# Kernel optimization log

Measured on AMD Instinct MI355X. Metric: run time of the kernel, lower is better.

The kernel has to match this reference:

```python
import jax, jax.numpy as jnp
import numpy as np

TOP_K = 8


def setup_inputs() -> dict:
    key = jax.random.key(0)
    k1, k2 = jax.random.split(key)
    N, D, E = 16384, 4096, 64
    x = jax.random.normal(k1, (N, D), dtype=jnp.float32)
    W = jax.random.normal(k2, (E, D), dtype=jnp.float32) * (1.0 / np.sqrt(D))
    b = jnp.zeros((E,), dtype=jnp.float32)
    return {"x": x, "W": W, "b": b}


def reference(x, W, b):
    # gate: [N, E]
    logits = jnp.einsum('nd,ed->ne', x, W) + b
    top_vals, top_idx = jax.lax.top_k(logits, TOP_K)  # [N, k]
    N = logits.shape[0]
    rows = jnp.arange(N)[:, None]  # [N, 1] broadcast against [N, k]
    neg_inf = jnp.full_like(logits, -jnp.inf)
    sparse = neg_inf.at[rows, top_idx].set(top_vals)
    sparse_logits = jax.nn.softmax(sparse, axis=-1)  # non-topk entries -> 0
    return (sparse_logits, top_idx)
```

## Files before the change

### kernel.cpp

```cpp
#include <hip/hip_runtime.h>
#include <cfloat>
#include <cmath>

#define M     16384
#define K     4096
#define E     64
#define TOPK  8
#define GAP_THRESH 1e-4f

#define RCAP  2048
#define FKS   8

typedef __attribute__((ext_vector_type(8))) short bf16x8;
typedef __attribute__((ext_vector_type(4))) short s16x4;
typedef __attribute__((ext_vector_type(4))) float f32x4;


__device__ __forceinline__ short f2bf(float f) {
    unsigned u = __builtin_bit_cast(unsigned, f);
    u += 0x7FFFu + ((u >> 16) & 1u);
    return (short)(u >> 16);
}
__device__ __forceinline__ float bf2f(short h) {
    unsigned u = ((unsigned)(unsigned short)h) << 16;
    return __builtin_bit_cast(float, u);
}

__global__ __launch_bounds__(256) void prep_kernel(const float* __restrict__ W,
                                                   short* __restrict__ Whf,
                                                   short* __restrict__ Wlf,
                                                   int* __restrict__ count) {
    int t = blockIdx.x * 256 + threadIdx.x;
    float w = W[t];
    short h = f2bf(w);
    short lo = f2bf(w - bf2f(h));
    int e = t >> 12, k = t & 4095;
    int gc = k >> 5, kk = k & 31;
    size_t fidx = (((size_t)gc * 4 + (e >> 4)) * 64 + (kk >> 3) * 16 + (e & 15)) * 8
                  + (kk & 7);
    Whf[fidx] = h;
    Wlf[fidx] = lo;
    if (t == 0) *count = 0;
}

__device__ __forceinline__ void mfma3(const bf16x8& ah, const bf16x8& al,
                                      const bf16x8& wh, const bf16x8& wl,
                                      f32x4& acc) {
    acc = __builtin_amdgcn_mfma_f32_16x16x32_bf16(ah, wh, acc, 0, 0, 0);
    acc = __builtin_amdgcn_mfma_f32_16x16x32_bf16(ah, wl, acc, 0, 0, 0);
    acc = __builtin_amdgcn_mfma_f32_16x16x32_bf16(al, wh, acc, 0, 0, 0);
}

__global__ __launch_bounds__(256) void gate_kernel(
    const float* __restrict__ x,
    const short* __restrict__ Whf,
    const short* __restrict__ Wlf,
    const float* __restrict__ b,
    float* __restrict__ outp,
    float* __restrict__ outi,
    int*   __restrict__ count,
    int*   __restrict__ list)
{
    __shared__ short lxh[2][16 * 128];
    __shared__ short lxl[2][16 * 128];
    __shared__ float llog[16 * E];

    const int t  = threadIdx.x;
    const int l  = t & 63;
    const int wv = t >> 6;
    const int row0 = blockIdx.x * 16;

    const int srA  = t >> 5;
    const int scol = t & 31;
    const float* gxA = x + (size_t)(row0 + srA) * K + scol * 4;
    const float* gxB = x + (size_t)(row0 + 8 + srA) * K + scol * 4;
    const int pu   = (scol >> 1) ^ (srA & 7);
    const int offA = srA * 128 + pu * 8 + (scol & 1) * 4;
    const int offB = (8 + srA) * 128 + pu * 8 + (scol & 1) * 4;

#define CVTW(nb, v, off) do {                                          \
        s16x4 hh_, ll_;                                                \
        float vv_[4] = {(v).x, (v).y, (v).z, (v).w};                   \
        _Pragma("unroll")                                              \
        for (int j_ = 0; j_ < 4; ++j_) {                               \
            short h_ = f2bf(vv_[j_]);                                  \
            hh_[j_] = h_;                                              \
            ll_[j_] = f2bf(vv_[j_] - bf2f(h_));                        \
        }                                                              \
        *reinterpret_cast<s16x4*>(&lxh[nb][off]) = hh_;                \
        *reinterpret_cast<s16x4*>(&lxl[nb][off]) = ll_;                \
    } while (0)

    int aoff[4];
#pragma unroll
    for (int q = 0; q < 4; ++q) {
        const int r = l & 15;
        const int u = q * 4 + (l >> 4);
        aoff[q] = r * 128 + (u ^ (r & 7)) * 8;
    }

    const short* ph = Whf + (size_t)wv * 512 + (size_t)l * 8;
    const short* pw = Wlf + (size_t)wv * 512 + (size_t)l * 8;

    f32x4 acc = {0, 0, 0, 0};

    {
        float4 a0 = *reinterpret_cast<const float4*>(gxA);
        float4 b0 = *reinterpret_cast<const float4*>(gxB);
        CVTW(0, a0, offA);
        CVTW(0, b0, offB);
    }
    __syncthreads();

    bf16x8 whA = *reinterpret_cast<const bf16x8*>(ph);
    bf16x8 wlA = *reinterpret_cast<const bf16x8*>(pw);
    bf16x8 whB, wlB;

    for (int sc = 0; sc < 32; ++sc) {
        const int buf = sc & 1;
        float4 sA, sB;
        if (sc + 1 < 32) {
            sA = *reinterpret_cast<const float4*>(gxA + (sc + 1) * 128);
            sB = *reinterpret_cast<const float4*>(gxB + (sc + 1) * 128);
        }

        const short* xh = lxh[buf];
        const short* xl = lxl[buf];
        const int c0 = sc * 4;

        whB = *reinterpret_cast<const bf16x8*>(ph + (size_t)(c0 + 1) * 2048);
        wlB = *reinterpret_cast<const bf16x8*>(pw + (size_t)(c0 + 1) * 2048);
        {
            bf16x8 ah = *reinterpret_cast<const bf16x8*>(&xh[aoff[0]]);
            bf16x8 al = *reinterpret_cast<const bf16x8*>(&xl[aoff[0]]);
            mfma3(ah, al, whA, wlA, acc);
        }
        whA = *reinterpret_cast<const bf16x8*>(ph + (size_t)(c0 + 2) * 2048);
        wlA = *reinterpret_cast<const bf16x8*>(pw + (size_t)(c0 + 2) * 2048);
        {
            bf16x8 ah = *reinterpret_cast<const bf16x8*>(&xh[aoff[1]]);
            bf16x8 al = *reinterpret_cast<const bf16x8*>(&xl[aoff[1]]);
            mfma3(ah, al, whB, wlB, acc);
        }
        whB = *reinterpret_cast<const bf16x8*>(ph + (size_t)(c0 + 3) * 2048);
        wlB = *reinterpret_cast<const bf16x8*>(pw + (size_t)(c0 + 3) * 2048);
        {
            bf16x8 ah = *reinterpret_cast<const bf16x8*>(&xh[aoff[2]]);
            bf16x8 al = *reinterpret_cast<const bf16x8*>(&xl[aoff[2]]);
            mfma3(ah, al, whA, wlA, acc);
        }
        if (c0 + 4 < 128) {
            whA = *reinterpret_cast<const bf16x8*>(ph + (size_t)(c0 + 4) * 2048);
            wlA = *reinterpret_cast<const bf16x8*>(pw + (size_t)(c0 + 4) * 2048);
        }
        {
            bf16x8 ah = *reinterpret_cast<const bf16x8*>(&xh[aoff[3]]);
            bf16x8 al = *reinterpret_cast<const bf16x8*>(&xl[aoff[3]]);
            mfma3(ah, al, whB, wlB, acc);
        }

        __syncthreads();
        if (sc + 1 < 32) {
            CVTW(buf ^ 1, sA, offA);
            CVTW(buf ^ 1, sB, offB);
        }
        __syncthreads();
    }
#undef CVTW

#pragma unroll
    for (int r = 0; r < 4; ++r)
        llog[((l >> 4) * 4 + r) * E + wv * 16 + (l & 15)] = acc[r];
    __syncthreads();

    const float bv = b[l];
#pragma unroll 1
    for (int rr = 0; rr < 4; ++rr) {
        const int rloc = wv * 4 + rr;
        const int row  = row0 + rloc;
        const float orig = llog[rloc * E + l] + bv;

        float cur = orig;
        float vals[9];
        float myidxf = 0.0f;
        bool  sel = false;

#pragma unroll
        for (int i = 0; i < 9; ++i) {
            float m = cur;
#pragma unroll
            for (int off = 32; off > 0; off >>= 1)
                m = fmaxf(m, __shfl_xor(m, off, 64));
            unsigned long long msk = __ballot(cur == m);
            int il = __ffsll((long long)msk) - 1;
            vals[i] = m;
            if (l == il) { cur = -FLT_MAX; if (i < TOPK) sel = true; }
            if (i < TOPK && l == i) myidxf = (float)il;
        }

        float ssum = 0.0f;
#pragma unroll
        for (int i = 0; i < TOPK; ++i) ssum += expf(vals[i] - vals[0]);
        float p = sel ? (expf(orig - vals[0]) / ssum) : 0.0f;

        outp[(size_t)row * E + l] = p;
        if (l < TOPK) outi[(size_t)row * TOPK + l] = myidxf;

        float mingap = FLT_MAX;
#pragma unroll
        for (int i = 0; i < 8; ++i) mingap = fminf(mingap, vals[i] - vals[i + 1]);
        if (l == 0 && mingap < GAP_THRESH) {
            int pos = atomicAdd(count, 1);
            if (pos < M) list[pos] = row;
        }
    }
}

__global__ __launch_bounds__(256) void fix1_kernel(
    const float* __restrict__ x,
    const float* __restrict__ W,
    double* __restrict__ dsum,
    const int* __restrict__ count,
    const int* __restrict__ list)
{
    __shared__ float xsl[512];
    const int t   = threadIdx.x;
    const int l   = t & 63;
    const int wv  = t >> 6;
    const int tot = min(*count, RCAP) * FKS;

    for (int p = blockIdx.x; p < tot; p += gridDim.x) {
        const int i   = p >> 3;
        const int ks  = p & 7;
        const int row = list[i];
        const int k0  = ks << 9;

        if (t < 128)
            reinterpret_cast<float4*>(xsl)[t] =
                reinterpret_cast<const float4*>(x + (size_t)row * K + k0)[t];
        __syncthreads();

        const float4* xs4 = reinterpret_cast<const float4*>(xsl);

#pragma unroll
        for (int g = 0; g < 2; ++g) {
            const int e0 = wv * 16 + g * 8;
            float4 w0[8], w1[8];
#pragma unroll
            for (int e8 = 0; e8 < 8; ++e8) {
                const float4* wp = reinterpret_cast<const float4*>(
                    W + (size_t)(e0 + e8) * K + k0);
                w0[e8] = wp[l];
                w1[e8] = wp[l + 64];
            }
            float4 xv0 = xs4[l];
            float4 xv1 = xs4[l + 64];

            double s[8];
#pragma unroll
            for (int e8 = 0; e8 < 8; ++e8) {
                double a = 0.0;
                a = fma((double)xv0.x, (double)w0[e8].x, a);
                a = fma((double)xv0.y, (double)w0[e8].y, a);
                a = fma((double)xv0.z, (double)w0[e8].z, a);
                a = fma((double)xv0.w, (double)w0[e8].w, a);
                a = fma((double)xv1.x, (double)w1[e8].x, a);
                a = fma((double)xv1.y, (double)w1[e8].y, a);
                a = fma((double)xv1.z, (double)w1[e8].z, a);
                a = fma((double)xv1.w, (double)w1[e8].w, a);
                s[e8] = a;
            }

#pragma unroll
            for (int e8 = 0; e8 < 8; ++e8) {
                double v = s[e8];
#pragma unroll
                for (int off = 32; off > 0; off >>= 1)
                    v += __shfl_xor(v, off, 64);
                if (l == 0)
                    dsum[((size_t)i * FKS + ks) * E + e0 + e8] = v;
            }
        }
        __syncthreads();
    }
}

__global__ __launch_bounds__(64) void fix2_kernel(
    const double* __restrict__ dsum,
    const float*  __restrict__ b,
    float* __restrict__ outp,
    float* __restrict__ outi,
    const int* __restrict__ count,
    const int* __restrict__ list)
{
    const int l   = threadIdx.x;
    const int cnt = min(*count, RCAP);

    for (int i = blockIdx.x; i < cnt; i += gridDim.x) {
        const int row = list[i];

        double orig = (double)b[l];
#pragma unroll
        for (int ks = 0; ks < FKS; ++ks)
            orig += dsum[((size_t)i * FKS + ks) * E + l];

        double cur = orig;
        double vals[TOPK];
        float  myidxf = 0.0f;
        bool   sel = false;

#pragma unroll
        for (int tt = 0; tt < TOPK; ++tt) {
            double m = cur;
#pragma unroll
            for (int off = 32; off > 0; off >>= 1) {
                double o = __shfl_xor(m, off, 64);
                m = fmax(m, o);
            }
            unsigned long long msk = __ballot(cur == m);
            int il = __ffsll((long long)msk) - 1;
            vals[tt] = m;
            if (l == il) { cur = -DBL_MAX; sel = true; }
            if (l == tt)  myidxf = (float)il;
        }

        double ssum = 0.0;
#pragma unroll
        for (int tt = 0; tt < TOPK; ++tt) ssum += exp(vals[tt] - vals[0]);
        float p = sel ? (float)(exp(orig - vals[0]) / ssum) : 0.0f;

        outp[(size_t)row * E + l] = p;
        if (l < TOPK) outi[(size_t)row * TOPK + l] = myidxf;
    }
}

__global__ __launch_bounds__(64) void fallback_kernel(
    const float* __restrict__ x,
    const float* __restrict__ W,
    const float* __restrict__ b,
    float* __restrict__ outp,
    float* __restrict__ outi)
{
    const int row = blockIdx.x * 64 + threadIdx.x;
    double lg[64];
#pragma unroll
    for (int e = 0; e < 64; ++e) lg[e] = (double)b[e];
    const float* xr = x + (size_t)row * K;
    for (int k = 0; k < K; k += 4) {
        float4 xa = *reinterpret_cast<const float4*>(xr + k);
        double xd[4] = {(double)xa.x, (double)xa.y, (double)xa.z, (double)xa.w};
#pragma unroll
        for (int e = 0; e < 64; ++e) {
            const float* wp = W + (size_t)e * K + k;
            double a = lg[e];
#pragma unroll
            for (int j = 0; j < 4; ++j) a = fma(xd[j], (double)wp[j], a);
            lg[e] = a;
        }
    }
    unsigned long long selm = 0ull;
    double vals[TOPK]; int idx[TOPK];
#pragma unroll
    for (int i = 0; i < TOPK; ++i) {
        double m = -DBL_MAX; int mi = 0;
#pragma unroll
        for (int e = 0; e < 64; ++e) {
            bool gt = !((selm >> e) & 1ull) && (lg[e] > m);
            m = gt ? lg[e] : m; mi = gt ? e : mi;
        }
        vals[i] = m; idx[i] = mi; selm |= (1ull << mi);
    }
    double ssum = 0.0;
#pragma unroll
    for (int i = 0; i < TOPK; ++i) ssum += exp(vals[i] - vals[0]);
    double inv = 1.0 / ssum;
#pragma unroll
    for (int e = 0; e < 64; ++e)
        outp[(size_t)row * E + e] =
            ((selm >> e) & 1ull) ? (float)(exp(lg[e] - vals[0]) * inv) : 0.0f;
#pragma unroll
    for (int i = 0; i < TOPK; ++i)
        outi[(size_t)row * TOPK + i] = (float)idx[i];
}

extern "C" void kernel_launch(void* const* d_in, const int* in_sizes, int n_in,
                              void* d_out, int out_size, void* d_ws, size_t ws_size,
                              hipStream_t stream) {
    (void)in_sizes; (void)n_in; (void)out_size;
    const float* x = (const float*)d_in[0];
    const float* W = (const float*)d_in[1];
    const float* b = (const float*)d_in[2];

    float* outp = (float*)d_out;
    float* outi = outp + (size_t)M * E;

    const size_t wh_off   = 0;
    const size_t wl_off   = wh_off + sizeof(short) * (size_t)E * K;
    const size_t cnt_off  = wl_off + sizeof(short) * (size_t)E * K;
    const size_t list_off = cnt_off + 256;
    const size_t dsum_off = list_off + (size_t)M * sizeof(int);
    const size_t need     = dsum_off + (size_t)RCAP * FKS * E * sizeof(double);

    if (ws_size >= need) {
        short*  Whf  = (short*)((char*)d_ws + wh_off);
        short*  Wlf  = (short*)((char*)d_ws + wl_off);
        int*    cnt  = (int*)((char*)d_ws + cnt_off);
        int*    list = (int*)((char*)d_ws + list_off);
        double* dsum = (double*)((char*)d_ws + dsum_off);

        prep_kernel<<<(E * K) / 256, 256, 0, stream>>>(W, Whf, Wlf, cnt);
        gate_kernel<<<M / 16, 256, 0, stream>>>(x, Whf, Wlf, b, outp, outi, cnt, list);
        fix1_kernel<<<4096, 256, 0, stream>>>(x, W, dsum, cnt, list);
        fix2_kernel<<<1024, 64, 0, stream>>>(dsum, b, outp, outi, cnt, list);
    } else {
        fallback_kernel<<<M / 64, 64, 0, stream>>>(x, W, b, outp, outi);
    }
}
```

Before: 107.2 us.

## Process 32 rows per block to reuse W fragments across two row tiles

Each block of the gate kernel now handles 32 token rows instead of 16. Every wave keeps two accumulators and applies each loaded W hi/lo fragment to two 16-row x tiles, which halves the W global/L2 traffic per row and doubles MFMA work per load. The cost is twice the LDS footprint, more registers, half as many blocks (512 on a 256-CU part), and a longer serial top-k epilogue of 8 rows per wave.

```diff
diff --git a/kernel.cpp b/kernel.cpp
--- a/kernel.cpp
+++ b/kernel.cpp
@@ -61,22 +61,23 @@
     int*   __restrict__ count,
     int*   __restrict__ list)
 {
-    __shared__ short lxh[2][16 * 128];
-    __shared__ short lxl[2][16 * 128];
-    __shared__ float llog[16 * E];
+    __shared__ short lxh[2][32 * 128];
+    __shared__ short lxl[2][32 * 128];
+    __shared__ float llog[32 * E];
 
     const int t  = threadIdx.x;
     const int l  = t & 63;
     const int wv = t >> 6;
-    const int row0 = blockIdx.x * 16;
+    const int row0 = blockIdx.x * 32;
 
     const int srA  = t >> 5;
     const int scol = t & 31;
-    const float* gxA = x + (size_t)(row0 + srA) * K + scol * 4;
-    const float* gxB = x + (size_t)(row0 + 8 + srA) * K + scol * 4;
-    const int pu   = (scol >> 1) ^ (srA & 7);
-    const int offA = srA * 128 + pu * 8 + (scol & 1) * 4;
-    const int offB = (8 + srA) * 128 + pu * 8 + (scol & 1) * 4;
+    const float* gx0 = x + (size_t)(row0 + srA) * K + scol * 4;
+    const int pu  = (scol >> 1) ^ (srA & 7);
+    const int sb  = pu * 8 + (scol & 1) * 4;
+    int offs[4];
+#pragma unroll
+    for (int j = 0; j < 4; ++j) offs[j] = (srA + 8 * j) * 128 + sb;
 
 #define CVTW(nb, v, off) do {                                          \
         s16x4 hh_, ll_;                                                \
@@ -91,6 +92,12 @@
         *reinterpret_cast<s16x4*>(&lxl[nb][off]) = ll_;                \
     } while (0)
 
+#define STAGE_LOAD(sc1)                                                \
+        float4 s0 = *reinterpret_cast<const float4*>(gx0 + (sc1) * 128);             \
+        float4 s1 = *reinterpret_cast<const float4*>(gx0 + (size_t)8  * K + (sc1) * 128); \
+        float4 s2 = *reinterpret_cast<const float4*>(gx0 + (size_t)16 * K + (sc1) * 128); \
+        float4 s3 = *reinterpret_cast<const float4*>(gx0 + (size_t)24 * K + (sc1) * 128)
+
     int aoff[4];
 #pragma unroll
     for (int q = 0; q < 4; ++q) {
@@ -102,13 +109,15 @@
     const short* ph = Whf + (size_t)wv * 512 + (size_t)l * 8;
     const short* pw = Wlf + (size_t)wv * 512 + (size_t)l * 8;
 
-    f32x4 acc = {0, 0, 0, 0};
+    f32x4 acc0 = {0, 0, 0, 0};
+    f32x4 acc1 = {0, 0, 0, 0};
 
     {
-        float4 a0 = *reinterpret_cast<const float4*>(gxA);
-        float4 b0 = *reinterpret_cast<const float4*>(gxB);
-        CVTW(0, a0, offA);
-        CVTW(0, b0, offB);
+        STAGE_LOAD(0);
+        CVTW(0, s0, offs[0]);
+        CVTW(0, s1, offs[1]);
+        CVTW(0, s2, offs[2]);
+        CVTW(0, s3, offs[3]);
     }
     __syncthreads();
 
@@ -118,65 +127,65 @@
 
     for (int sc = 0; sc < 32; ++sc) {
         const int buf = sc & 1;
-        float4 sA, sB;
+        float4 p0, p1, p2, p3;
         if (sc + 1 < 32) {
-            sA = *reinterpret_cast<const float4*>(gxA + (sc + 1) * 128);
-            sB = *reinterpret_cast<const float4*>(gxB + (sc + 1) * 128);
+            STAGE_LOAD(sc + 1);
+            p0 = s0; p1 = s1; p2 = s2; p3 = s3;
         }
 
         const short* xh = lxh[buf];
         const short* xl = lxl[buf];
         const int c0 = sc * 4;
 
+#define DOCHUNK(WH, WL, q)                                             \
+        {                                                              \
+            bf16x8 ah = *reinterpret_cast<const bf16x8*>(&xh[aoff[q]]);        \
+            bf16x8 al = *reinterpret_cast<const bf16x8*>(&xl[aoff[q]]);        \
+            mfma3(ah, al, WH, WL, acc0);                               \
+            bf16x8 ah2 = *reinterpret_cast<const bf16x8*>(&xh[aoff[q] + 2048]); \
+            bf16x8 al2 = *reinterpret_cast<const bf16x8*>(&xl[aoff[q] + 2048]); \
+            mfma3(ah2, al2, WH, WL, acc1);                             \
+        }
+
         whB = *reinterpret_cast<const bf16x8*>(ph + (size_t)(c0 + 1) * 2048);
         wlB = *reinterpret_cast<const bf16x8*>(pw + (size_t)(c0 + 1) * 2048);
-        {
-            bf16x8 ah = *reinterpret_cast<const bf16x8*>(&xh[aoff[0]]);
-            bf16x8 al = *reinterpret_cast<const bf16x8*>(&xl[aoff[0]]);
-            mfma3(ah, al, whA, wlA, acc);
-        }
+        DOCHUNK(whA, wlA, 0)
         whA = *reinterpret_cast<const bf16x8*>(ph + (size_t)(c0 + 2) * 2048);
         wlA = *reinterpret_cast<const bf16x8*>(pw + (size_t)(c0 + 2) * 2048);
-        {
-            bf16x8 ah = *reinterpret_cast<const bf16x8*>(&xh[aoff[1]]);
-            bf16x8 al = *reinterpret_cast<const bf16x8*>(&xl[aoff[1]]);
-            mfma3(ah, al, whB, wlB, acc);
-        }
+        DOCHUNK(whB, wlB, 1)
         whB = *reinterpret_cast<const bf16x8*>(ph + (size_t)(c0 + 3) * 2048);
         wlB = *reinterpret_cast<const bf16x8*>(pw + (size_t)(c0 + 3) * 2048);
-        {
-            bf16x8 ah = *reinterpret_cast<const bf16x8*>(&xh[aoff[2]]);
-            bf16x8 al = *reinterpret_cast<const bf16x8*>(&xl[aoff[2]]);
-            mfma3(ah, al, whA, wlA, acc);
-        }
+        DOCHUNK(whA, wlA, 2)
         if (c0 + 4 < 128) {
             whA = *reinterpret_cast<const bf16x8*>(ph + (size_t)(c0 + 4) * 2048);
             wlA = *reinterpret_cast<const bf16x8*>(pw + (size_t)(c0 + 4) * 2048);
         }
-        {
-            bf16x8 ah = *reinterpret_cast<const bf16x8*>(&xh[aoff[3]]);
-            bf16x8 al = *reinterpret_cast<const bf16x8*>(&xl[aoff[3]]);
-            mfma3(ah, al, whB, wlB, acc);
-        }
+        DOCHUNK(whB, wlB, 3)
+#undef DOCHUNK
 
         __syncthreads();
         if (sc + 1 < 32) {
-            CVTW(buf ^ 1, sA, offA);
-            CVTW(buf ^ 1, sB, offB);
+            CVTW(buf ^ 1, p0, offs[0]);
+            CVTW(buf ^ 1, p1, offs[1]);
+            CVTW(buf ^ 1, p2, offs[2]);
+            CVTW(buf ^ 1, p3, offs[3]);
         }
         __syncthreads();
     }
 #undef CVTW
-
-#pragma unroll
-    for (int r = 0; r < 4; ++r)
-        llog[((l >> 4) * 4 + r) * E + wv * 16 + (l & 15)] = acc[r];
+#undef STAGE_LOAD
+
+#pragma unroll
+    for (int r = 0; r < 4; ++r) {
+        llog[((l >> 4) * 4 + r) * E + wv * 16 + (l & 15)] = acc0[r];
+        llog[(16 + (l >> 4) * 4 + r) * E + wv * 16 + (l & 15)] = acc1[r];
+    }
     __syncthreads();
 
     const float bv = b[l];
 #pragma unroll 1
-    for (int rr = 0; rr < 4; ++rr) {
-        const int rloc = wv * 4 + rr;
+    for (int rr = 0; rr < 8; ++rr) {
+        const int rloc = wv * 8 + rr;
         const int row  = row0 + rloc;
         const float orig = llog[rloc * E + l] + bv;
 
@@ -409,7 +418,7 @@
         double* dsum = (double*)((char*)d_ws + dsum_off);
 
         prep_kernel<<<(E * K) / 256, 256, 0, stream>>>(W, Whf, Wlf, cnt);
-        gate_kernel<<<M / 16, 256, 0, stream>>>(x, Whf, Wlf, b, outp, outi, cnt, list);
+        gate_kernel<<<M / 32, 256, 0, stream>>>(x, Whf, Wlf, b, outp, outi, cnt, list);
         fix1_kernel<<<4096, 256, 0, stream>>>(x, W, dsum, cnt, list);
         fix2_kernel<<<1024, 64, 0, stream>>>(dsum, b, outp, outi, cnt, list);
     } else {
```

After: 118.4 us. +10.5%, slower.
